# Kernel tuning notes

Hardware: AMD Instinct MI355X
Metric: run time of the kernel (lower is better)

The kernel has to match this reference:

```python
import jax, jax.numpy as jnp
import numpy as np
import math

B, S, H, A = 16, 2048, 1024, 64
SCALE = math.sqrt(A)

def setup_inputs() -> dict:
    key = jax.random.key(0)
    ks = jax.random.split(key, 8)
    x = jax.random.normal(ks[0], (B, S, H), dtype=jnp.float32)
    mask = jax.random.randint(ks[1], (B, S), 0, 2).astype(jnp.int32)
    Wq = jax.random.normal(ks[2], (H, A), dtype=jnp.float32) / math.sqrt(H)
    bq = jnp.zeros((A,), dtype=jnp.float32)
    Wk = jax.random.normal(ks[3], (H, A), dtype=jnp.float32) / math.sqrt(H)
    bk = jnp.zeros((A,), dtype=jnp.float32)
    Wv = jax.random.normal(ks[4], (H, H), dtype=jnp.float32) / math.sqrt(H)
    bv = jnp.zeros((H,), dtype=jnp.float32)
    return {"x": x, "mask": mask, "Wq": Wq, "bq": bq, "Wk": Wk, "bk": bk, "Wv": Wv, "bv": bv}

def reference(x, mask, Wq, bq, Wk, bk, Wv, bv):
    # x: (B,S,H), mask: (B,S) int {0,1}
    Q = x @ Wq + bq            # (B,S,A)
    K = x @ Wk + bk            # (B,S,A)
    V = x @ Wv + bv            # (B,S,H)
    scores = jnp.einsum('bsa,bta->bst', Q, K) / SCALE  # (B,S,S)
    scores = jnp.where(mask[:, None, :] == 0, -jnp.inf, scores)
    attn = jax.nn.softmax(scores, axis=-1)
    attn = jnp.nan_to_num(attn, nan=0.0)  # rows fully masked -> 0
    context = jnp.einsum('bst,bth->bsh', attn, V)      # (B,S,H)
    m = mask[:, :, None].astype(context.dtype)          # (B,S,1)
    context = context * m
    output = context.sum(axis=1) / (m.sum(axis=1) + 1e-8)  # (B,H)
    return output, attn.mean(axis=1)                    # (B,H), (B,S)
```

## Files before the change

### kernel.cpp

```cpp
#include <hip/hip_runtime.h>
#include <math.h>

#define BN_ 16
#define SS  2048
#define HH  1024

typedef unsigned short u16;
typedef unsigned int   u32;
typedef __bf16 bf16x8 __attribute__((ext_vector_type(8)));
typedef float  f32x4  __attribute__((ext_vector_type(4)));
typedef float  f32x16 __attribute__((ext_vector_type(16)));
#define MFMA16 __builtin_amdgcn_mfma_f32_16x16x32_bf16
#define MFMA32 __builtin_amdgcn_mfma_f32_32x32x16_bf16

#define QK_OFF    0
#define QK_FLOATS (BN_*SS*64)
#define WT_OFF    (QK_OFF + QK_FLOATS)
#define WT_FLOATS (64*HH)
#define CP_OFF    (WT_OFF + WT_FLOATS)
#define CP_FLOATS (BN_*32*2*SS)
#define NB_OFF    (CP_OFF + CP_FLOATS)
#define NBW_OFF   (NB_OFF + 16)
#define U_OFF     (NBW_OFF + 16)

__device__ __forceinline__ u16 f2b(float f) {
    unsigned u = __builtin_bit_cast(unsigned, f);
    return (u16)((u + 0x7FFFu + ((u >> 16) & 1u)) >> 16);
}

__device__ __forceinline__ bf16x8 cvt8(float4 a, float4 b) {
    bf16x8 r;
    r[0] = (__bf16)a.x; r[1] = (__bf16)a.y; r[2] = (__bf16)a.z; r[3] = (__bf16)a.w;
    r[4] = (__bf16)b.x; r[5] = (__bf16)b.y; r[6] = (__bf16)b.z; r[7] = (__bf16)b.w;
    return r;
}

__device__ __forceinline__ int swze(int row, int e) {
    return row * 64 + (e ^ ((row & 7) << 3));
}

__device__ __forceinline__ bf16x8 ldfrag(const u16* t, int row16, int ks, int l6) {
    int row = row16 + (l6 & 15);
    int e = ks * 32 + ((l6 >> 4) << 3);
    return *(const bf16x8*)&t[swze(row, e)];
}

__device__ __forceinline__ void gload16(const u16* g, u16* l) {
    __builtin_amdgcn_global_load_lds(
        (const __attribute__((address_space(1))) u32*)g,
        (__attribute__((address_space(3))) u32*)l, 16, 0, 0);
}

__global__ __launch_bounds__(256) void k_prep(const float* __restrict__ Wq,
                                              const float* __restrict__ Wk,
                                              const int* __restrict__ mask,
                                              u16* __restrict__ wt,
                                              float* __restrict__ nbv,
                                              float* __restrict__ nbw,
                                              float* __restrict__ u,
                                              float* __restrict__ outz) {
    int bid = blockIdx.x, tid = threadIdx.x;
    if (bid < 128) {
        const float* src = (bid < 64) ? &Wq[bid] : &Wk[bid - 64];
        for (int k = tid; k < HH; k += 256)
            wt[(size_t)bid * HH + k] = f2b(src[(size_t)k * 64]);
    } else if (bid < 144) {
        int b = bid - 128;
        int s = 0;
        for (int i = tid; i < SS; i += 256) s += mask[b * SS + i];
        float fs = (float)s;
        for (int off = 1; off < 64; off <<= 1) fs += __shfl_xor(fs, off);
        __shared__ float red[4];
        if ((tid & 63) == 0) red[tid >> 6] = fs;
        __syncthreads();
        if (tid == 0) {
            float t = red[0] + red[1] + red[2] + red[3];
            nbv[b] = t + 1e-8f;
            nbw[b] = t / (t + 1e-8f);
        }
    } else {
        int zb = bid - 144;
        float* dst = (zb < 8) ? (u + zb * 2048) : (outz + (zb - 8) * 2048);
        for (int i = tid; i < 2048; i += 256) dst[i] = 0.f;
    }
}

__global__ __launch_bounds__(256) void k_qkproj(const float* __restrict__ x,
                                                const u16* __restrict__ wt,
                                                const float* __restrict__ bq,
                                                const float* __restrict__ bk,
                                                u16* __restrict__ qk) {
    __shared__ __align__(16) u16 Bs0[128 * 64];
    __shared__ __align__(16) u16 Bs1[128 * 64];
    int tid = threadIdx.x, l6 = tid & 63, w = tid >> 6;
    int lr = l6 & 15, lk = l6 >> 4;
    int row = blockIdx.x * 64 + w * 16;
    const float* xr = x + (size_t)(row + lr) * HH + lk * 8;
    int r0 = tid >> 3, j = tid & 7;
    const u16* bsrc = wt + (size_t)r0 * HH + (j ^ (r0 & 7)) * 8;
    float4 x0, x1, x2, x3;
    #define GLOADB(kt, B_) { const u16* s_ = bsrc + (kt) * 64; u16* l_ = B_ + tid * 8;  \
        gload16(s_,            l_);        gload16(s_ + 32 * HH, l_ + 2048);            \
        gload16(s_ + 64 * HH,  l_ + 4096); gload16(s_ + 96 * HH, l_ + 6144); }
    #define LOADA(kt) { const float* p_ = xr + (kt) * 64;                               \
        x0 = *(const float4*)p_;        x1 = *(const float4*)(p_ + 4);                  \
        x2 = *(const float4*)(p_ + 32); x3 = *(const float4*)(p_ + 36); }

    f32x4 acc[8];
    #pragma unroll
    for (int jj = 0; jj < 8; ++jj) acc[jj] = (f32x4){0.f, 0.f, 0.f, 0.f};

    GLOADB(0, Bs0); LOADA(0);
    __syncthreads();
    for (int kt = 0; kt < 16; ++kt) {
        const u16* Bs = (kt & 1) ? Bs1 : Bs0;
        bf16x8 a0 = cvt8(x0, x1);
        bf16x8 a1 = cvt8(x2, x3);
        if (kt < 15) {
            if (kt & 1) { GLOADB(kt + 1, Bs0); } else { GLOADB(kt + 1, Bs1); }
            LOADA(kt + 1);
        }
        __builtin_amdgcn_s_setprio(1);
        #pragma unroll
        for (int jj = 0; jj < 8; ++jj) {
            bf16x8 b0 = ldfrag(Bs, jj * 16, 0, l6);
            bf16x8 b1 = ldfrag(Bs, jj * 16, 1, l6);
            acc[jj] = MFMA16(a0, b0, acc[jj], 0, 0, 0);
            acc[jj] = MFMA16(a1, b1, acc[jj], 0, 0, 0);
        }
        __builtin_amdgcn_s_setprio(0);
        if (kt < 15) __syncthreads();
    }
    #pragma unroll
    for (int jj = 0; jj < 8; ++jj) {
        int n = jj * 16 + lr;
        float bias = (n < 64) ? bq[n] : bk[n - 64];
        int mrow = row + lk * 4;
        #pragma unroll
        for (int r4 = 0; r4 < 4; ++r4)
            qk[(size_t)(mrow + r4) * 128 + n] = f2b(acc[jj][r4] + bias);
    }
    #undef GLOADB
    #undef LOADA
}

__global__ __launch_bounds__(256) void k_score(const u16* __restrict__ qk,
                                               const int* __restrict__ mask,
                                               float* __restrict__ cpart) {
    __shared__ __align__(16) u16 Ks0[128 * 64];
    __shared__ __align__(16) u16 Ks1[128 * 64];
    __shared__ float pml[SS];
    __shared__ float redbuf[4][64];
    __shared__ float lshs[64];
    int l = blockIdx.x;
    int b = (l & 7) * 2 + ((l >> 3) >> 5);
    int sb = (l >> 3) & 31;
    int tid = threadIdx.x, l6 = tid & 63, w = tid >> 6;
    int cl = l6 & 31, hi = l6 >> 5;
    for (int i = tid; i < SS; i += 256) pml[i] = mask[b * SS + i] ? 0.f : -1e30f;
    const u16* qkb = qk + (size_t)b * SS * 128;
    int q0 = sb * 64;
    bf16x8 qA[2][4];
    #pragma unroll
    for (int rs = 0; rs < 2; ++rs)
        #pragma unroll
        for (int ks = 0; ks < 4; ++ks)
            qA[rs][ks] = *(const bf16x8*)&qkb[(size_t)(q0 + rs * 32 + cl) * 128 + ks * 16 + hi * 8];
    int r0 = tid >> 3, j = tid & 7;
    const u16* ksrc = qkb + 64 + (size_t)r0 * 128 + (j ^ (r0 & 7)) * 8;
    #define GLOADK(tt, B_) { const u16* s_ = ksrc + (size_t)(tt) * (128 * 128); u16* l_ = B_ + tid * 8; \
        gload16(s_,             l_);        gload16(s_ + 32 * 128, l_ + 2048);                          \
        gload16(s_ + 64 * 128,  l_ + 4096); gload16(s_ + 96 * 128, l_ + 6144); }

    const float SCL = 0.18033688f;
    GLOADK(0, Ks0);
    __syncthreads();
    float rsum[2][16];
    #pragma unroll
    for (int rs = 0; rs < 2; ++rs)
        #pragma unroll
        for (int r = 0; r < 16; ++r) rsum[rs][r] = 0.f;
    for (int tt = 0; tt < 16; ++tt) {
        const u16* Ks = (tt & 1) ? Ks1 : Ks0;
        if (tt < 15) {
            if (tt & 1) { GLOADK(tt + 1, Ks0); } else { GLOADK(tt + 1, Ks1); }
        }
        bf16x8 kB[4];
        #pragma unroll
        for (int ks = 0; ks < 4; ++ks)
            kB[ks] = *(const bf16x8*)&Ks[swze(w * 32 + cl, ks * 16 + hi * 8)];
        float pmv = pml[tt * 128 + w * 32 + cl];
        __builtin_amdgcn_s_setprio(1);
        #pragma unroll
        for (int rs = 0; rs < 2; ++rs) {
            f32x16 acc = {};
            #pragma unroll
            for (int ks = 0; ks < 4; ++ks) acc = MFMA32(qA[rs][ks], kB[ks], acc, 0, 0, 0);
            #pragma unroll
            for (int r = 0; r < 16; ++r)
                rsum[rs][r] += exp2f(fmaf(acc[r], SCL, pmv));
        }
        __builtin_amdgcn_s_setprio(0);
        if (tt < 15) __syncthreads();
    }
    #pragma unroll
    for (int off = 1; off < 32; off <<= 1)
        #pragma unroll
        for (int rs = 0; rs < 2; ++rs)
            #pragma unroll
            for (int r = 0; r < 16; ++r)
                rsum[rs][r] += __shfl_xor(rsum[rs][r], off);
    if (cl == 0) {
        #pragma unroll
        for (int rs = 0; rs < 2; ++rs)
            #pragma unroll
            for (int r = 0; r < 16; ++r)
                redbuf[w][rs * 32 + (r & 3) + 8 * (r >> 2) + 4 * hi] = rsum[rs][r];
    }
    GLOADK(0, Ks0);
    __syncthreads();
    if (tid < 64) {
        float lv = redbuf[0][tid] + redbuf[1][tid] + redbuf[2][tid] + redbuf[3][tid];
        lshs[tid] = (lv > 0.f) ? -log2f(lv) : -1e30f;
    }
    __syncthreads();
    float lsh[2][16];
    unsigned qmb = 0;
    #pragma unroll
    for (int rs = 0; rs < 2; ++rs)
        #pragma unroll
        for (int r = 0; r < 16; ++r) {
            int rowi = rs * 32 + (r & 3) + 8 * (r >> 2) + 4 * hi;
            lsh[rs][r] = lshs[rowi];
            qmb |= (pml[q0 + rowi] == 0.f ? 1u : 0u) << (rs * 16 + r);
        }
    for (int tt = 0; tt < 16; ++tt) {
        const u16* Ks = (tt & 1) ? Ks1 : Ks0;
        if (tt < 15) {
            if (tt & 1) { GLOADK(tt + 1, Ks0); } else { GLOADK(tt + 1, Ks1); }
        }
        bf16x8 kB[4];
        #pragma unroll
        for (int ks = 0; ks < 4; ++ks)
            kB[ks] = *(const bf16x8*)&Ks[swze(w * 32 + cl, ks * 16 + hi * 8)];
        float pmv = pml[tt * 128 + w * 32 + cl];
        float sa = 0.f, sm = 0.f;
        __builtin_amdgcn_s_setprio(1);
        #pragma unroll
        for (int rs = 0; rs < 2; ++rs) {
            f32x16 acc = {};
            #pragma unroll
            for (int ks = 0; ks < 4; ++ks) acc = MFMA32(qA[rs][ks], kB[ks], acc, 0, 0, 0);
            #pragma unroll
            for (int r = 0; r < 16; ++r) {
                float e = exp2f(fmaf(acc[r], SCL, lsh[rs][r]) + pmv);
                sa += e;
                sm += ((qmb >> (rs * 16 + r)) & 1u) ? e : 0.f;
            }
        }
        __builtin_amdgcn_s_setprio(0);
        sa += __shfl_xor(sa, 32);
        sm += __shfl_xor(sm, 32);
        if (hi == 0) {
            size_t base = (((size_t)b * 32 + sb) * 2) * SS + tt * 128 + w * 32 + cl;
            cpart[base] = sa;
            cpart[base + SS] = sm;
        }
        if (tt < 15) __syncthreads();
    }
    #undef GLOADK
}

__global__ __launch_bounds__(256) void k_u(const float* __restrict__ x,
                                           const float* __restrict__ cpart,
                                           const int* __restrict__ mask,
                                           const float* __restrict__ nbv,
                                           float* __restrict__ u,
                                           float* __restrict__ out_mean) {
    __shared__ float wl[64];
    __shared__ float red2[2][4][64];
    int b = blockIdx.x, ch = blockIdx.y;
    int tid = threadIdx.x, tl = tid & 63, qd = tid >> 6;
    int t = ch * 64 + tl;
    float sa = 0.f, sm = 0.f;
    #pragma unroll
    for (int k = 0; k < 8; ++k) {
        const float* p = &cpart[(((size_t)b * 32 + (qd * 8 + k)) * 2) * SS + t];
        sa += p[0];
        sm += p[SS];
    }
    red2[0][qd][tl] = sa;
    red2[1][qd][tl] = sm;
    __syncthreads();
    if (tid < 64) {
        float sat = red2[0][0][tl] + red2[0][1][tl] + red2[0][2][tl] + red2[0][3][tl];
        float smt = red2[1][0][tl] + red2[1][1][tl] + red2[1][2][tl] + red2[1][3][tl];
        float pm = mask[b * SS + t] ? 1.f : 0.f;
        out_mean[b * SS + t] = sat * pm * (1.f / SS);
        wl[tl] = smt * pm / nbv[b];
    }
    __syncthreads();
    const float* xb = &x[((size_t)b * SS + ch * 64) * HH + tid * 4];
    float4 acc = {0.f, 0.f, 0.f, 0.f};
    #pragma unroll 16
    for (int tt = 0; tt < 64; ++tt) {
        float4 xv = *(const float4*)&xb[(size_t)tt * HH];
        float wv = wl[tt];
        acc.x += wv * xv.x; acc.y += wv * xv.y;
        acc.z += wv * xv.z; acc.w += wv * xv.w;
    }
    float* up = &u[(size_t)b * HH + tid * 4];
    atomicAdd(&up[0], acc.x);
    atomicAdd(&up[1], acc.y);
    atomicAdd(&up[2], acc.z);
    atomicAdd(&up[3], acc.w);
}

__global__ __launch_bounds__(256) void k_out0a(const float* __restrict__ u,
                                               const float* __restrict__ Wv,
                                               const float* __restrict__ bv,
                                               const float* __restrict__ nbw,
                                               float* __restrict__ out) {
    __shared__ float uT[64][16];
    __shared__ float red[4][64][16];
    int cb = blockIdx.x, hb = blockIdx.y;
    int c0 = cb * 64, h0 = hb * 64;
    int tid = threadIdx.x;
    int hl = tid & 63, cq = tid >> 6;
    #pragma unroll
    for (int it = 0; it < 4; ++it) {
        int b = it * 4 + cq;
        uT[hl][b] = u[(size_t)b * HH + c0 + hl];
    }
    __syncthreads();
    int h = h0 + hl;
    float acc[16];
    #pragma unroll
    for (int b = 0; b < 16; ++b) acc[b] = 0.f;
    #pragma unroll
    for (int cc = 0; cc < 16; ++cc) {
        int c = cq * 16 + cc;
        float wv = Wv[(size_t)(c0 + c) * HH + h];
        #pragma unroll
        for (int b = 0; b < 16; ++b) acc[b] += uT[c][b] * wv;
    }
    #pragma unroll
    for (int b = 0; b < 16; ++b) red[cq][hl][b] = acc[b];
    __syncthreads();
    #pragma unroll
    for (int it = 0; it < 4; ++it) {
        int b = it * 4 + cq;
        float s = red[0][hl][b] + red[1][hl][b] + red[2][hl][b] + red[3][hl][b];
        if (cb == 0) s += bv[h] * nbw[b];
        atomicAdd(&out[(size_t)b * HH + h], s);
    }
}

extern "C" void kernel_launch(void* const* d_in, const int* in_sizes, int n_in,
                              void* d_out, int out_size, void* d_ws, size_t ws_size,
                              hipStream_t stream) {
    const float* x  = (const float*)d_in[0];
    const int* mask = (const int*)d_in[1];
    const float* Wq = (const float*)d_in[2];
    const float* bq = (const float*)d_in[3];
    const float* Wk = (const float*)d_in[4];
    const float* bk = (const float*)d_in[5];
    const float* Wv = (const float*)d_in[6];
    const float* bv = (const float*)d_in[7];
    float* out = (float*)d_out;
    float* ws  = (float*)d_ws;

    u16*   qk    = (u16*)(ws + QK_OFF);
    u16*   wt    = (u16*)(ws + WT_OFF);
    float* cpart = ws + CP_OFF;
    float* nbv   = ws + NB_OFF;
    float* nbw   = ws + NBW_OFF;
    float* u     = ws + U_OFF;

    k_prep   <<<dim3(160),        dim3(256), 0, stream>>>(Wq, Wk, mask, wt, nbv, nbw, u, out);
    k_qkproj <<<dim3(512),        dim3(256), 0, stream>>>(x, wt, bq, bk, qk);
    k_score  <<<dim3(512),        dim3(256), 0, stream>>>(qk, mask, cpart);
    k_u      <<<dim3(BN_, 32),    dim3(256), 0, stream>>>(x, cpart, mask, nbv, u, out + BN_ * HH);
    k_out0a  <<<dim3(16, 16),     dim3(256), 0, stream>>>(u, Wv, bv, nbw, out);
}
```

Measured before the change: 129.3 us.

## Deepen QK projection pipeline to four LDS buffers, two k-tiles per barrier

The Q/K projection kernel moves from double-buffered to quad-buffered weight tiles in LDS and loads two k-tiles per iteration. It holds two x register sets, so there is one barrier per pair of k-steps. The aim is to halve synchronisation and keep more global loads in flight while the MFMAs run. In exchange, LDS use doubles to 64KB per block, which may lower occupancy, and register pressure rises.

```diff
diff --git a/kernel.cpp b/kernel.cpp
--- a/kernel.cpp
+++ b/kernel.cpp
@@ -90,46 +90,51 @@
                                                 const float* __restrict__ bq,
                                                 const float* __restrict__ bk,
                                                 u16* __restrict__ qk) {
-    __shared__ __align__(16) u16 Bs0[128 * 64];
-    __shared__ __align__(16) u16 Bs1[128 * 64];
+    __shared__ __align__(16) u16 Bs[4][128 * 64];
     int tid = threadIdx.x, l6 = tid & 63, w = tid >> 6;
     int lr = l6 & 15, lk = l6 >> 4;
     int row = blockIdx.x * 64 + w * 16;
     const float* xr = x + (size_t)(row + lr) * HH + lk * 8;
     int r0 = tid >> 3, j = tid & 7;
     const u16* bsrc = wt + (size_t)r0 * HH + (j ^ (r0 & 7)) * 8;
-    float4 x0, x1, x2, x3;
-    #define GLOADB(kt, B_) { const u16* s_ = bsrc + (kt) * 64; u16* l_ = B_ + tid * 8;  \
-        gload16(s_,            l_);        gload16(s_ + 32 * HH, l_ + 2048);            \
+    float4 xa0[4], xa1[4];
+    #define GLOADB(kt, BI) { const u16* s_ = bsrc + (kt) * 64; u16* l_ = Bs[BI] + tid * 8;  \
+        gload16(s_,            l_);        gload16(s_ + 32 * HH, l_ + 2048);                \
         gload16(s_ + 64 * HH,  l_ + 4096); gload16(s_ + 96 * HH, l_ + 6144); }
-    #define LOADA(kt) { const float* p_ = xr + (kt) * 64;                               \
-        x0 = *(const float4*)p_;        x1 = *(const float4*)(p_ + 4);                  \
-        x2 = *(const float4*)(p_ + 32); x3 = *(const float4*)(p_ + 36); }
+    #define LOADA(kt, A_) { const float* p_ = xr + (kt) * 64;                               \
+        A_[0] = *(const float4*)p_;        A_[1] = *(const float4*)(p_ + 4);                \
+        A_[2] = *(const float4*)(p_ + 32); A_[3] = *(const float4*)(p_ + 36); }
+    #define COMP(BI, A_) { const u16* Bp = Bs[BI];                                          \
+        bf16x8 a0 = cvt8(A_[0], A_[1]);                                                     \
+        bf16x8 a1 = cvt8(A_[2], A_[3]);                                                     \
+        _Pragma("unroll")                                                                   \
+        for (int jj = 0; jj < 8; ++jj) {                                                    \
+            bf16x8 b0 = ldfrag(Bp, jj * 16, 0, l6);                                         \
+            bf16x8 b1 = ldfrag(Bp, jj * 16, 1, l6);                                         \
+            acc[jj] = MFMA16(a0, b0, acc[jj], 0, 0, 0);                                     \
+            acc[jj] = MFMA16(a1, b1, acc[jj], 0, 0, 0);                                     \
+        } }
 
     f32x4 acc[8];
     #pragma unroll
     for (int jj = 0; jj < 8; ++jj) acc[jj] = (f32x4){0.f, 0.f, 0.f, 0.f};
 
-    GLOADB(0, Bs0); LOADA(0);
-    __syncthreads();
-    for (int kt = 0; kt < 16; ++kt) {
-        const u16* Bs = (kt & 1) ? Bs1 : Bs0;
-        bf16x8 a0 = cvt8(x0, x1);
-        bf16x8 a1 = cvt8(x2, x3);
-        if (kt < 15) {
-            if (kt & 1) { GLOADB(kt + 1, Bs0); } else { GLOADB(kt + 1, Bs1); }
-            LOADA(kt + 1);
-        }
+    GLOADB(0, 0); GLOADB(1, 1); LOADA(0, xa0); LOADA(1, xa1);
+    __syncthreads();
+    for (int p = 0; p < 8; ++p) {
+        int k0 = 2 * p;
+        if (p < 7) { GLOADB(k0 + 2, (k0 + 2) & 3); GLOADB(k0 + 3, (k0 + 3) & 3); }
         __builtin_amdgcn_s_setprio(1);
-        #pragma unroll
-        for (int jj = 0; jj < 8; ++jj) {
-            bf16x8 b0 = ldfrag(Bs, jj * 16, 0, l6);
-            bf16x8 b1 = ldfrag(Bs, jj * 16, 1, l6);
-            acc[jj] = MFMA16(a0, b0, acc[jj], 0, 0, 0);
-            acc[jj] = MFMA16(a1, b1, acc[jj], 0, 0, 0);
-        }
+        COMP(k0 & 3, xa0);
         __builtin_amdgcn_s_setprio(0);
-        if (kt < 15) __syncthreads();
+        if (p < 7) LOADA(k0 + 2, xa0);
+        __builtin_amdgcn_s_setprio(1);
+        COMP((k0 + 1) & 3, xa1);
+        __builtin_amdgcn_s_setprio(0);
+        if (p < 7) {
+            LOADA(k0 + 3, xa1);
+            __syncthreads();
+        }
     }
     #pragma unroll
     for (int jj = 0; jj < 8; ++jj) {
@@ -142,6 +147,7 @@
     }
     #undef GLOADB
     #undef LOADA
+    #undef COMP
 }
 
 __global__ __launch_bounds__(256) void k_score(const u16* __restrict__ qk,
```

New measurement: 127.4 us, median of 3. Within noise of the previous version (-1.5%).
